# Kernel optimization log

Measured on AMD Instinct MI355X. Metric: run time of the kernel, lower is better.

## Reference

```python
import jax, jax.numpy as jnp
import numpy as np

B, P, H, W = 8, 128, 32, 32
NC = 4                 # num_classes = NUM_REL_GROUP + 1
DOBJ = 4424            # 2*DOBJ = 8848
CIN = 256
C = 128 + 8848         # 8976 GCN channel dim


def setup_inputs() -> dict:
    key = jax.random.key(0)
    ks = jax.random.split(key, 24)
    s = 0.02  # weight scale to keep activations moderate
    inp = {
        "x": jax.random.normal(ks[0], (B, CIN, H, W), jnp.float32),
        "rel_pair_idxs": jax.random.randint(ks[1], (B, P, 2), 0, 640, dtype=jnp.int32),
        "obj_rep": jax.random.normal(ks[2], (640, DOBJ), jnp.float32),
        # ADD_GCN params
        "fc_w": jax.random.normal(ks[3], (NC, CIN), jnp.float32) * s,
        "ct_w": jax.random.normal(ks[4], (128, CIN), jnp.float32) * s,
        "ct_b": jnp.zeros((128,), jnp.float32),
        # DynamicGraphConvolution params
        "A": jax.random.normal(ks[5], (NC, NC), jnp.float32) * 0.25,          # static_adj conv1d (no bias)
        "sw_w": jax.random.normal(ks[6], (C, C), jnp.float32) * s / np.sqrt(C) * 30,
        "sw_b": jnp.zeros((C,), jnp.float32),
        "cg_w": jax.random.normal(ks[7], (C, C), jnp.float32) * s / np.sqrt(C) * 30,
        "cg_b": jnp.zeros((C,), jnp.float32),
        "bn_g": jnp.ones((C,), jnp.float32),
        "bn_b": jnp.zeros((C,), jnp.float32),
        "bn_m": jnp.zeros((C,), jnp.float32),
        "bn_v": jnp.ones((C,), jnp.float32),
        "co_w": jax.random.normal(ks[8], (NC, 2 * C), jnp.float32) * s / np.sqrt(C) * 30,
        "co_b": jnp.zeros((NC,), jnp.float32),
        "dw_w": jax.random.normal(ks[9], (C, C), jnp.float32) * s / np.sqrt(C) * 30,
        "dw_b": jnp.zeros((C,), jnp.float32),
        "ll_w": jax.random.normal(ks[10], (NC, C), jnp.float32) * s / np.sqrt(C) * 30,
        "ll_b": jnp.zeros((NC,), jnp.float32),
        "mask_mat": jnp.eye(NC, dtype=jnp.float32),
    }
    return inp


def reference(x, rel_pair_idxs, obj_rep, fc_w, ct_w, ct_b, A, sw_w, sw_b,
              cg_w, cg_b, bn_g, bn_b, bn_m, bn_v, co_w, co_b, dw_w, dw_b,
              ll_w, ll_b, mask_mat):
    leaky = lambda t: jax.nn.leaky_relu(t, 0.2)
    b, cin, h, w = x.shape
    xr = x.reshape(b, cin, h * w)                                  # (B,256,HW)

    # forward_classification_sm: fc -> topk(1).mean == max over spatial
    y = jnp.einsum('oc,bcs->bos', fc_w, xr)                        # (B,NC,HW)
    out1 = y.max(-1)                                               # (B,NC)

    # forward_sam
    mask = jax.nn.sigmoid(y)                                       # (B,NC,HW)
    v = jnp.einsum('oc,bcs->bos', ct_w, xr) + ct_b[None, :, None]  # (B,128,HW)
    v = jnp.einsum('bcs,bns->bcn', v, mask)                        # (B,128,NC)

    # pairwise object features (gather), tiled over NC node slots
    o1 = obj_rep[rel_pair_idxs[..., 0]]                            # (B,P,DOBJ)
    o2 = obj_rep[rel_pair_idxs[..., 1]]
    pf = jnp.concatenate([o1, o2], -1)                             # (B,P,8848)
    p = pf.shape[1]
    pf = jnp.broadcast_to(pf[..., None], pf.shape + (NC,))         # (B,P,8848,NC)
    vb = jnp.broadcast_to(v[:, None], (b, p) + v.shape[1:])        # (B,P,128,NC)
    g = jnp.concatenate([pf, vb], 2).reshape(b * p, C, NC)         # (BP,C,NC)

    # --- DynamicGraphConvolution ---
    # static GCN: node-mix conv1d (no bias) + leaky, then channel 1x1 conv + leaky
    xs = leaky(jnp.einsum('nm,pcm->pcn', A, g))                    # (BP,C,NC)
    xs = leaky(jnp.einsum('oc,pcn->pon', sw_w, xs) + sw_b[None, :, None])
    hg = g + xs

    # dynamic adjacency
    glb = hg.mean(-1)                                              # (BP,C) gap
    glb = glb @ cg_w.T + cg_b                                      # conv_global (1x1)
    glb = (glb - bn_m) * jax.lax.rsqrt(bn_v + 1e-5) * bn_g + bn_b  # BN (eval)
    glb = leaky(glb)
    # conv_create_co_mat over cat([glb_expand, hg], ch) without materializing cat
    adj = jax.nn.sigmoid(
        jnp.einsum('oc,pc->po', co_w[:, :C], glb)[:, :, None]
        + jnp.einsum('oc,pcn->pon', co_w[:, C:], hg)
        + co_b[None, :, None])                                     # (BP,NC,NC)

    # dynamic GCN
    hd = leaky(jnp.einsum('pcn,pnm->pcm', hg, adj))
    z = leaky(jnp.einsum('oc,pcn->pon', dw_w, hd) + dw_b[None, :, None])  # (BP,C,NC)

    # head: last_linear + leaky, masked diagonal sum
    out2 = leaky(jnp.einsum('oc,pcn->pon', ll_w, z) + ll_b[None, :, None])  # (BP,NC,NC)
    out2 = (out2 * jax.lax.stop_gradient(mask_mat)).sum(-1)        # (BP,NC)

    o1b = jnp.broadcast_to(out1[:, None], (b, p, NC)).reshape(b * p, NC)
    return ((o1b + out2) * 0.5).reshape(b, p, NC)
```

## Files before the change

kernel.cpp:

```cpp
#include <hip/hip_runtime.h>
#include <stdint.h>

#define DEVI __device__ __forceinline__

typedef unsigned short u16;
typedef __bf16 bf16x8 __attribute__((ext_vector_type(8)));
typedef float f32x4 __attribute__((ext_vector_type(4)));
typedef u16 u16x8 __attribute__((ext_vector_type(8)));

DEVI u16 f2bf(float f){
  union { float f; unsigned u; } v; v.f = f;
  unsigned r = v.u + 0x7FFFu + ((v.u >> 16) & 1u);
  return (u16)(r >> 16);
}
DEVI float bf2f(u16 h){
  union { unsigned u; float f; } v; v.u = ((unsigned)h) << 16;
  return v.f;
}
DEVI float lky(float t){ return t > 0.f ? t : 0.2f * t; }

#define GLD16(gp, lp) __builtin_amdgcn_global_load_lds( \
    (const __attribute__((address_space(1))) void*)(gp), \
    (__attribute__((address_space(3))) void*)(lp), 16, 0, 0)


DEVI void stage_half(const u16* __restrict__ G, size_t grow0, int kcol, int Kp,
                     u16* lds, int t)
{
  #pragma unroll
  for (int j = 0; j < 2; ++j){
    const int off16 = j*512 + t;
    const int rl = off16 >> 3, sl = off16 & 7;
    const u16* gp = G + (grow0 + rl)*(size_t)Kp + kcol + ((sl ^ (rl & 7))*8);
    GLD16(gp, lds + off16*8);
  }
}

template<int RB, int RA>
DEVI void ph_reads(const u16* __restrict__ Ab, const u16* __restrict__ Bb,
                   bf16x8 (&afr)[4][2], bf16x8 (&bfr)[4][2],
                   int wr, int wc, int l4, int l15)
{
  if constexpr (RA >= 0){
    #pragma unroll
    for (int m = 0; m < 4; ++m){
      const int r = wr*128 + RA*64 + m*16 + l15;
      afr[m][0] = *(const bf16x8*)&Ab[r*64 + (((0+l4) ^ (r & 7))*8)];
      afr[m][1] = *(const bf16x8*)&Ab[r*64 + (((4+l4) ^ (r & 7))*8)];
    }
  }
  if constexpr (RB >= 0){
    #pragma unroll
    for (int nn = 0; nn < 2; ++nn){
      const int r = wc*64 + (RB+nn)*16 + l15;
      bfr[RB+nn][0] = *(const bf16x8*)&Bb[r*64 + (((0+l4) ^ (r & 7))*8)];
      bfr[RB+nn][1] = *(const bf16x8*)&Bb[r*64 + (((4+l4) ^ (r & 7))*8)];
    }
  }
}

template<int MH, int NH, int VM>
DEVI void ph_mfma(bf16x8 (&afr)[4][2], bf16x8 (&bfr)[4][2], f32x4 (&acc)[8][4])
{
  __builtin_amdgcn_s_barrier();
  __builtin_amdgcn_s_setprio(1);
  #pragma unroll
  for (int m = 0; m < 4; ++m)
    #pragma unroll
    for (int nn = 0; nn < 2; ++nn)
      #pragma unroll
      for (int ks = 0; ks < 2; ++ks)
        acc[MH*4+m][NH+nn] = __builtin_amdgcn_mfma_f32_16x16x32_bf16(
            afr[m][ks], bfr[NH+nn][ks], acc[MH*4+m][NH+nn], 0, 0, 0);
  __builtin_amdgcn_s_setprio(0);
  if constexpr (VM == 4){
    asm volatile("s_waitcnt vmcnt(4)" ::: "memory");
  }
  __builtin_amdgcn_s_barrier();
}

template<int EPI>
__global__ __launch_bounds__(512, 2)
void gemm256(const u16* __restrict__ A, const u16* __restrict__ B,
             int Kp, int Nt, int SN, int Mreal, float* __restrict__ C, long long ldc,
             const float* __restrict__ bias, const float* __restrict__ scale,
             const float* __restrict__ off, const float* __restrict__ llw,
             float* __restrict__ oacc)
{
  __shared__ __align__(16) u16 As[2][16384];
  __shared__ __align__(16) u16 Bs[2][16384];
  const int t    = threadIdx.x;
  const int lane = t & 63;
  const int wid  = t >> 6;
  const int wr = wid >> 2, wc = wid & 3;
  const int l4 = lane >> 4, l15 = lane & 15;

  const int nwg = gridDim.x;
  const int xc = blockIdx.x & 7, pp = blockIdx.x >> 3;
  const int qq = nwg >> 3, rr = nwg & 7;
  const int wg = (xc < rr ? xc*(qq+1) : rr*(qq+1) + (xc-rr)*qq) + pp;
  const int strip_sz = (nwg / Nt) * SN;
  const int strip = wg / strip_sz, srem = wg % strip_sz;
  const int mt = srem / SN, nt = strip*SN + srem % SN;

  const size_t am0 = (size_t)mt*256;
  const size_t bn0 = (size_t)nt*256;

  f32x4 acc[8][4];
  #pragma unroll
  for (int i = 0; i < 8; ++i)
    #pragma unroll
    for (int j = 0; j < 4; ++j) acc[i][j] = f32x4{0.f,0.f,0.f,0.f};
  bf16x8 afr[4][2], bfr[4][2];

  const int NT2 = Kp >> 6;
  const int NI  = NT2 >> 1;

  stage_half(A, am0+0,   0,  Kp, &As[0][0],    t);
  stage_half(A, am0+128, 0,  Kp, &As[0][8192], t);
  stage_half(B, bn0+0,   0,  Kp, &Bs[0][0],    t);
  stage_half(B, bn0+128, 0,  Kp, &Bs[0][8192], t);
  stage_half(B, bn0+0,   64, Kp, &Bs[1][0],    t);
  stage_half(B, bn0+128, 64, Kp, &Bs[1][8192], t);
  asm volatile("s_waitcnt vmcnt(4)" ::: "memory");
  __builtin_amdgcn_s_barrier();

  for (int i = 0; i < NI; ++i){
    const int k1  = 2*i + 1;
    const int ts0 = (2*i+2 < NT2) ? 2*i+2 : 2*i;
    const int ts1 = (2*i+3 < NT2) ? 2*i+3 : 2*i+1;
    ph_reads<0,0>(&As[0][0], &Bs[0][0], afr, bfr, wr, wc, l4, l15);
    stage_half(A, am0+0,   k1*64,  Kp, &As[1][0],    t);
    ph_mfma<0,0,-1>(afr, bfr, acc);
    ph_reads<2,-1>(&As[0][0], &Bs[0][0], afr, bfr, wr, wc, l4, l15);
    stage_half(A, am0+128, k1*64,  Kp, &As[1][8192], t);
    ph_mfma<0,2,-1>(afr, bfr, acc);
    ph_reads<-1,1>(&As[0][0], &Bs[0][0], afr, bfr, wr, wc, l4, l15);
    stage_half(B, bn0+0,   ts0*64, Kp, &Bs[0][0],    t);
    ph_mfma<1,2,-1>(afr, bfr, acc);
    stage_half(B, bn0+128, ts0*64, Kp, &Bs[0][8192], t);
    ph_mfma<1,0,4>(afr, bfr, acc);
    ph_reads<0,0>(&As[1][0], &Bs[1][0], afr, bfr, wr, wc, l4, l15);
    stage_half(A, am0+0,   ts0*64, Kp, &As[0][0],    t);
    ph_mfma<0,0,-1>(afr, bfr, acc);
    ph_reads<2,-1>(&As[1][0], &Bs[1][0], afr, bfr, wr, wc, l4, l15);
    stage_half(A, am0+128, ts0*64, Kp, &As[0][8192], t);
    ph_mfma<0,2,-1>(afr, bfr, acc);
    ph_reads<-1,1>(&As[1][0], &Bs[1][0], afr, bfr, wr, wc, l4, l15);
    stage_half(B, bn0+0,   ts1*64, Kp, &Bs[1][0],    t);
    ph_mfma<1,2,-1>(afr, bfr, acc);
    stage_half(B, bn0+128, ts1*64, Kp, &Bs[1][8192], t);
    ph_mfma<1,0,4>(afr, bfr, acc);
  }
  asm volatile("s_waitcnt vmcnt(0)" ::: "memory");

  const int ob0 = mt*256 + wr*128;
  const int nb0 = nt*256 + wc*64;

  if (EPI == 0){
    #pragma unroll
    for (int mi = 0; mi < 8; ++mi){
      const int ob = ob0 + mi*16 + l4*4;
      if (ob < Mreal){
        #pragma unroll
        for (int ni = 0; ni < 4; ++ni){
          const int n = nb0 + ni*16 + l15;
          *(f32x4*)&C[(size_t)n*ldc + ob] = acc[mi][ni];
        }
      }
    }
  } else if (EPI == 2){
    #pragma unroll
    for (int mi = 0; mi < 8; ++mi){
      const int ob = ob0 + mi*16 + l4*4;
      if (ob < Mreal){
        const float sc0=scale[ob],sc1=scale[ob+1],sc2=scale[ob+2],sc3=scale[ob+3];
        const float of0=off[ob],of1=off[ob+1],of2=off[ob+2],of3=off[ob+3];
        #pragma unroll
        for (int ni = 0; ni < 4; ++ni){
          const int n = nb0 + ni*16 + l15;
          f32x4 a = acc[mi][ni];
          f32x4 vv = { lky(a[0]*sc0+of0), lky(a[1]*sc1+of1),
                       lky(a[2]*sc2+of2), lky(a[3]*sc3+of3) };
          *(f32x4*)&C[(size_t)n*ldc + ob] = vv;
        }
      }
    }
  } else {
    #pragma unroll
    for (int ni = 0; ni < 4; ++ni){
      float s0=0.f, s1=0.f, s2=0.f, s3=0.f;
      #pragma unroll
      for (int mi = 0; mi < 8; ++mi){
        #pragma unroll
        for (int r = 0; r < 4; ++r){
          const int o = ob0 + mi*16 + l4*4 + r;
          if (o < Mreal){
            const float val = lky(acc[mi][ni][r] + bias[o]);
            s0 += llw[o]         * val;
            s1 += llw[8976 + o]  * val;
            s2 += llw[17952 + o] * val;
            s3 += llw[26928 + o] * val;
          }
        }
      }
      const int n = nb0 + ni*16 + l15;
      const int q = n >> 2, m = n & 3;
      float sv[4] = {s0,s1,s2,s3};
      #pragma unroll
      for (int o4 = 0; o4 < 4; ++o4){
        float tt = sv[o4];
        tt += __shfl_xor(tt, 16);
        tt += __shfl_xor(tt, 32);
        if (l4 == 0) atomicAdd(&oacc[(q*4 + o4)*4 + m], tt);
      }
    }
  }
}

__global__ __launch_bounds__(256)
void gemm_vpre(const u16* __restrict__ A, const u16* __restrict__ B,
               int Kp, int Nt, int Mreal, float* __restrict__ C, long long ldc,
               const float* __restrict__ bias)
{
  __shared__ __align__(16) u16 As[2][4096];
  __shared__ __align__(16) u16 Bs[2][4096];
  const int tid  = threadIdx.x;
  const int lane = tid & 63;
  const int wr   = (tid >> 6) >> 1, wc = (tid >> 6) & 1;
  const int l4   = lane >> 4, l15 = lane & 15;
  const int mt   = blockIdx.x / Nt, nt = blockIdx.x % Nt;

  const size_t arow = (size_t)(mt*128 + (tid>>2)) * Kp + (tid&3)*8;
  const size_t brow = (size_t)(nt*128 + (tid>>2)) * Kp + (tid&3)*8;
  const int    ldst = (tid>>2)*32 + (tid&3)*8;
  const size_t rowskip = (size_t)64 * Kp;

  f32x4 acc[4][4];
  #pragma unroll
  for (int i=0;i<4;i++)
    #pragma unroll
    for (int j=0;j<4;j++) acc[i][j] = f32x4{0.f,0.f,0.f,0.f};

  const int NT = Kp >> 5;
  {
    const u16* a0 = A + arow; const u16* b0 = B + brow;
    GLD16(a0,           &As[0][ldst]);
    GLD16(a0 + rowskip, &As[0][ldst + 2048]);
    GLD16(b0,           &Bs[0][ldst]);
    GLD16(b0 + rowskip, &Bs[0][ldst + 2048]);
  }
  __syncthreads();

  for (int kt=0; kt<NT; ++kt){
    const int cur = kt & 1;
    if (kt + 1 < NT){
      const u16* a0 = A + arow + (size_t)(kt+1)*32;
      const u16* b0 = B + brow + (size_t)(kt+1)*32;
      GLD16(a0,           &As[cur^1][ldst]);
      GLD16(a0 + rowskip, &As[cur^1][ldst + 2048]);
      GLD16(b0,           &Bs[cur^1][ldst]);
      GLD16(b0 + rowskip, &Bs[cur^1][ldst + 2048]);
    }
    bf16x8 af[4], bf[4];
    #pragma unroll
    for (int mi=0;mi<4;mi++)
      af[mi] = *(const bf16x8*)&As[cur][(wr*64 + mi*16 + l15)*32 + l4*8];
    #pragma unroll
    for (int ni=0;ni<4;ni++)
      bf[ni] = *(const bf16x8*)&Bs[cur][(wc*64 + ni*16 + l15)*32 + l4*8];
    #pragma unroll
    for (int mi=0;mi<4;mi++)
      #pragma unroll
      for (int ni=0;ni<4;ni++)
        acc[mi][ni] = __builtin_amdgcn_mfma_f32_16x16x32_bf16(af[mi], bf[ni], acc[mi][ni], 0, 0, 0);
    __syncthreads();
  }

  const int ob0 = mt*128 + wr*64;
  const int nb0 = nt*128 + wc*64;
  #pragma unroll
  for (int mi=0;mi<4;mi++)
    #pragma unroll
    for (int r=0;r<4;r++){
      const int o = ob0 + mi*16 + l4*4 + r;
      if (o < Mreal){
        const float bb = bias[o];
        #pragma unroll
        for (int ni=0;ni<4;ni++){
          const int n = nb0 + ni*16 + l15;
          C[(size_t)o*ldc + n] = acc[mi][ni][r] + bb;
        }
      }
    }
}

__global__ void k_cvt_pad(const float* __restrict__ src, int srows, int scols,
                          int lds_, int koff, u16* __restrict__ dst, int Kp)
{
  const int r = blockIdx.x;
  const int nch = Kp >> 3;
  for (int ch = threadIdx.x; ch < nch; ch += blockDim.x){
    const int k = ch*8;
    u16 o[8];
    if (r < srows){
      #pragma unroll
      for (int i=0;i<8;i++){
        const int kk = k + i;
        o[i] = (kk < scols) ? f2bf(src[(size_t)r*lds_ + koff + kk]) : (u16)0;
      }
    } else {
      #pragma unroll
      for (int i=0;i<8;i++) o[i] = 0;
    }
    u16x8 vv = { o[0],o[1],o[2],o[3],o[4],o[5],o[6],o[7] };
    *(u16x8*)&dst[(size_t)r*Kp + k] = vv;
  }
}

__global__ void k_cvt_sww(const float* __restrict__ src, u16* __restrict__ dst)
{
  const int r = blockIdx.x;
  const float* row = src + (size_t)r*8976;
  u16* d1 = dst + (size_t)r*4480;
  u16* d2 = dst + (size_t)(8976+r)*4480;
  for (int ch = threadIdx.x; ch < 560; ch += 256){
    const int k = ch*8;
    u16 a[8], b[8];
    #pragma unroll
    for (int i=0;i<8;i++){
      const int kk = k+i;
      a[i] = (kk < 4424) ? f2bf(row[kk])        : (u16)0;
      b[i] = (kk < 4424) ? f2bf(row[4424 + kk]) : (u16)0;
    }
    u16x8 va = { a[0],a[1],a[2],a[3],a[4],a[5],a[6],a[7] };
    u16x8 vb = { b[0],b[1],b[2],b[3],b[4],b[5],b[6],b[7] };
    *(u16x8*)&d1[k] = va;
    *(u16x8*)&d2[k] = vb;
  }
}

__global__ void k_cvt_obj(const float* __restrict__ obj, u16* __restrict__ dst)
{
  const int r = blockIdx.x;
  const int ab = (r >= 640);
  const float* src = obj + (size_t)(ab ? r-640 : r)*4424;
  for (int ch = threadIdx.x; ch < 560; ch += 256){
    const int k = ch*8;
    u16 o[8];
    #pragma unroll
    for (int i=0;i<8;i++){
      const int kk = k+i;
      float f = (kk < 4424) ? src[kk] : 0.f;
      if (ab) f = fabsf(f);
      o[i] = f2bf(f);
    }
    u16x8 vv = { o[0],o[1],o[2],o[3],o[4],o[5],o[6],o[7] };
    *(u16x8*)&dst[(size_t)r*4480 + k] = vv;
  }
}

__global__ void k_xT(const float* __restrict__ x, u16* __restrict__ xT)
{
  __shared__ float t[32][33];
  const int bid = blockIdx.x;
  const int b = bid >> 8; const int cs = (bid >> 5) & 7; const int ss = bid & 31;
  const int tx = threadIdx.x & 31, ty = threadIdx.x >> 5;
  #pragma unroll
  for (int i=0;i<4;i++){
    const int r = ty + i*8;
    t[r][tx] = x[((size_t)(b*256 + cs*32 + r))*1024 + ss*32 + tx];
  }
  __syncthreads();
  #pragma unroll
  for (int i=0;i<4;i++){
    const int r = ty + i*8;
    xT[((size_t)(b*1024 + ss*32 + r))*256 + cs*32 + tx] = f2bf(t[tx][r]);
  }
}

__global__ void k_ymask(const float* __restrict__ x, const float* __restrict__ fcw,
                        float* __restrict__ y, float* __restrict__ mask)
{
  __shared__ float fc[1024];
  const int b = blockIdx.x >> 2, st = blockIdx.x & 3;
  for (int i=threadIdx.x; i<1024; i+=256) fc[i] = fcw[i];
  __syncthreads();
  const int s = st*256 + threadIdx.x;
  float a0=0,a1=0,a2=0,a3=0;
  for (int c=0;c<256;c++){
    const float xv = x[((size_t)(b*256+c))*1024 + s];
    a0 += fc[c]*xv; a1 += fc[256+c]*xv; a2 += fc[512+c]*xv; a3 += fc[768+c]*xv;
  }
  const size_t base = (size_t)(b*4)*1024 + s;
  y[base]        = a0; mask[base]        = 1.f/(1.f+expf(-a0));
  y[base+1024]   = a1; mask[base+1024]   = 1.f/(1.f+expf(-a1));
  y[base+2048]   = a2; mask[base+2048]   = 1.f/(1.f+expf(-a2));
  y[base+3072]   = a3; mask[base+3072]   = 1.f/(1.f+expf(-a3));
}

__global__ void k_out1(const float* __restrict__ y, float* __restrict__ out1){
  const int bn = blockIdx.x;
  float m = -3.4e38f;
  for (int s=threadIdx.x; s<1024; s+=256) m = fmaxf(m, y[(size_t)bn*1024+s]);
  for (int o=32;o;o>>=1) m = fmaxf(m, __shfl_xor(m,o));
  __shared__ float red[4];
  if ((threadIdx.x&63)==0) red[threadIdx.x>>6] = m;
  __syncthreads();
  if (threadIdx.x==0) out1[bn] = fmaxf(fmaxf(red[0],red[1]),fmaxf(red[2],red[3]));
}

__global__ void k_v(const float* __restrict__ vpreT, const float* __restrict__ mask,
                    float* __restrict__ v){
  const int b = blockIdx.x >> 7, j = blockIdx.x & 127;
  float a[4]={0,0,0,0};
  for (int s=threadIdx.x; s<1024; s+=256){
    const float pv = vpreT[(size_t)j*8192 + b*1024 + s];
    #pragma unroll
    for (int m=0;m<4;m++) a[m] += pv * mask[((size_t)(b*4+m))*1024 + s];
  }
  __shared__ float red[4][5];
  #pragma unroll
  for (int m=0;m<4;m++){
    float t=a[m];
    for (int o=32;o;o>>=1) t += __shfl_xor(t,o);
    if ((threadIdx.x&63)==0) red[m][threadIdx.x>>6]=t;
  }
  __syncthreads();
  if (threadIdx.x<4)
    v[(size_t)(b*128+j)*4 + threadIdx.x] =
      red[threadIdx.x][0]+red[threadIdx.x][1]+red[threadIdx.x][2]+red[threadIdx.x][3];
}

__global__ void k_lv(const float* __restrict__ Am, const float* __restrict__ v,
                     float* __restrict__ lv){
  const int idx = blockIdx.x*256 + threadIdx.x;
  if (idx < 1024){
    #pragma unroll
    for (int n=0;n<4;n++){
      float s=0;
      #pragma unroll
      for (int m=0;m<4;m++) s += Am[n*4+m]*v[idx*4+m];
      lv[idx*4+n] = lky(s);
    }
  }
}

__global__ void k_sV(const float* __restrict__ sw, const float* __restrict__ lv,
                     float* __restrict__ sV){
  __shared__ float l[4096];
  for (int i=threadIdx.x; i<4096; i+=256) l[i]=lv[i];
  __syncthreads();
  const int o = blockIdx.x*256 + threadIdx.x;
  if (o >= 8976) return;
  float acc[8][4] = {};
  const float* row = sw + (size_t)o*8976 + 8848;
  for (int j=0;j<128;j++){
    const float wv = row[j];
    #pragma unroll
    for (int b=0;b<8;b++){
      const float* lb = &l[(b*128+j)*4];
      #pragma unroll
      for (int n=0;n<4;n++) acc[b][n] += wv*lb[n];
    }
  }
  #pragma unroll
  for (int b=0;b<8;b++){
    f32x4 vv = {acc[b][0],acc[b][1],acc[b][2],acc[b][3]};
    *(f32x4*)&sV[((size_t)b*8976 + o)*4] = vv;
  }
}

__global__ void k_so(const float* __restrict__ cgb, const float* __restrict__ g,
                     const float* __restrict__ b2, const float* __restrict__ m,
                     const float* __restrict__ vvar, float* __restrict__ so){
  const int o = blockIdx.x*256+threadIdx.x;
  if (o<8976){
    const float sc = g[o]*rsqrtf(vvar[o]+1e-5f);
    so[o]=sc; so[8976+o] = (cgb[o]-m[o])*sc + b2[o];
  }
}

__global__ void k_glb_t2(const float* __restrict__ U, const float* __restrict__ obj,
                         const int* __restrict__ rel,
                         const float* __restrict__ sV, const float* __restrict__ swb,
                         const float* __restrict__ v, const float* __restrict__ Am,
                         const float* __restrict__ cow, u16* __restrict__ glbB,
                         float* __restrict__ t2)
{
  const int q = blockIdx.x; const int b = q >> 7;
  const int i1 = rel[q*2], i2 = rel[q*2+1];
  const float* u1  = U + (size_t)i1*17952;
  const float* u2  = U + (size_t)i2*17952 + 8976;
  const float* u1a = U + (size_t)(640+i1)*17952;
  const float* u2a = U + (size_t)(640+i2)*17952 + 8976;
  const float* o1 = obj + (size_t)i1*4424;
  const float* o2 = obj + (size_t)i2*4424;
  float rA[4], aA[4];
  #pragma unroll
  for (int n=0;n<4;n++){
    const float s = Am[n*4]+Am[n*4+1]+Am[n*4+2]+Am[n*4+3];
    rA[n]=0.6f*s; aA[n]=0.4f*fabsf(s);
  }
  float t2a[16] = {};
  for (int c = threadIdx.x; c < 9088; c += 256){
    if (c < 8976){
      const float p1 = u1[c] + u2[c];
      const float p2 = u1a[c] + u2a[c];
      const f32x4 sv = *(const f32x4*)&sV[((size_t)b*8976 + c)*4];
      const float sb = swb[c];
      const float gs = (c < 4424) ? o1[c] : (c < 8848) ? o2[c-4424] : 0.f;
      float hg[4]; float sum = 0.f;
      #pragma unroll
      for (int n=0;n<4;n++){
        const float xs2 = lky(rA[n]*p1 + aA[n]*p2 + sv[n] + sb);
        const float g = (c < 8848) ? gs : v[((size_t)b*128 + (c-8848))*4 + n];
        hg[n] = g + xs2; sum += hg[n];
      }
      glbB[(size_t)q*9088 + c] = f2bf(0.25f*sum);
      #pragma unroll
      for (int o4=0;o4<4;o4++){
        const float cw = cow[(size_t)o4*17952 + 8976 + c];
        #pragma unroll
        for (int n=0;n<4;n++) t2a[o4*4+n] += cw*hg[n];
      }
    } else {
      glbB[(size_t)q*9088 + c] = 0;
    }
  }
  __shared__ float red[16][5];
  #pragma unroll
  for (int i=0;i<16;i++){
    float t = t2a[i];
    for (int o=32;o;o>>=1) t += __shfl_xor(t,o);
    if ((threadIdx.x&63)==0) red[i][threadIdx.x>>6]=t;
  }
  __syncthreads();
  if (threadIdx.x < 16)
    t2[q*16+threadIdx.x] = red[threadIdx.x][0]+red[threadIdx.x][1]
                          +red[threadIdx.x][2]+red[threadIdx.x][3];
}

__global__ void k_adj(const float* __restrict__ glb2, const float* __restrict__ cow,
                      const float* __restrict__ t2, const float* __restrict__ cob,
                      float* __restrict__ adj)
{
  const int q = blockIdx.x;
  float a[4]={0,0,0,0};
  for (int c=threadIdx.x; c<8976; c+=256){
    const float g = glb2[(size_t)q*8976+c];
    #pragma unroll
    for (int o=0;o<4;o++) a[o] += cow[(size_t)o*17952 + c]*g;
  }
  __shared__ float red[4][5]; __shared__ float co1[4];
  #pragma unroll
  for (int i=0;i<4;i++){
    float t=a[i]; for (int o=32;o;o>>=1) t += __shfl_xor(t,o);
    if ((threadIdx.x&63)==0) red[i][threadIdx.x>>6]=t;
  }
  __syncthreads();
  if (threadIdx.x<4)
    co1[threadIdx.x]=red[threadIdx.x][0]+red[threadIdx.x][1]+red[threadIdx.x][2]+red[threadIdx.x][3];
  __syncthreads();
  if (threadIdx.x<16){
    const int a_=threadIdx.x>>2, m=threadIdx.x&3;
    const float t = co1[a_] + t2[q*16 + a_*4 + m] + cob[a_];
    adj[q*16 + a_*4 + m] = 1.f/(1.f+expf(-t));
  }
}

__global__ void k_hd(const float* __restrict__ U, const float* __restrict__ obj,
                     const int* __restrict__ rel,
                     const float* __restrict__ sV, const float* __restrict__ swb,
                     const float* __restrict__ v, const float* __restrict__ Am,
                     const float* __restrict__ adj, u16* __restrict__ hdb)
{
  const int q = blockIdx.x; const int b = q>>7;
  const int i1 = rel[q*2], i2 = rel[q*2+1];
  const float* u1  = U + (size_t)i1*17952;
  const float* u2  = U + (size_t)i2*17952 + 8976;
  const float* u1a = U + (size_t)(640+i1)*17952;
  const float* u2a = U + (size_t)(640+i2)*17952 + 8976;
  const float* o1 = obj + (size_t)i1*4424;
  const float* o2 = obj + (size_t)i2*4424;
  float rA[4], aA[4];
  #pragma unroll
  for (int n=0;n<4;n++){
    const float s = Am[n*4]+Am[n*4+1]+Am[n*4+2]+Am[n*4+3];
    rA[n]=0.6f*s; aA[n]=0.4f*fabsf(s);
  }
  __shared__ float aj[16];
  if (threadIdx.x<16) aj[threadIdx.x] = adj[q*16+threadIdx.x];
  __syncthreads();
  float ajr[16];
  #pragma unroll
  for (int i=0;i<16;i++) ajr[i]=aj[i];
  for (int c=threadIdx.x; c<9088; c+=256){
    if (c<8976){
      const float p1 = u1[c] + u2[c];
      const float p2 = u1a[c] + u2a[c];
      const f32x4 sv = *(const f32x4*)&sV[((size_t)b*8976 + c)*4];
      const float sb = swb[c];
      const float gs = (c < 4424) ? o1[c] : (c < 8848) ? o2[c-4424] : 0.f;
      float hg[4];
      #pragma unroll
      for (int n=0;n<4;n++){
        const float xs2 = lky(rA[n]*p1 + aA[n]*p2 + sv[n] + sb);
        const float g = (c < 8848) ? gs : v[((size_t)b*128 + (c-8848))*4 + n];
        hg[n] = g + xs2;
      }
      #pragma unroll
      for (int m=0;m<4;m++){
        const float hv = lky(hg[0]*ajr[m] + hg[1]*ajr[4+m] + hg[2]*ajr[8+m] + hg[3]*ajr[12+m]);
        hdb[((size_t)(q*4+m))*9088 + c] = f2bf(hv);
      }
    } else {
      #pragma unroll
      for (int m=0;m<4;m++) hdb[((size_t)(q*4+m))*9088 + c] = 0;
    }
  }
}

__global__ void k_final(const float* __restrict__ o2f, const float* __restrict__ out1,
                        const float* __restrict__ llb, const float* __restrict__ mm,
                        float* __restrict__ out)
{
  const int idx = blockIdx.x*256+threadIdx.x;
  if (idx < 4096){
    const int q = idx>>2, o = idx&3, b = q>>7;
    float s=0.f;
    #pragma unroll
    for (int m=0;m<4;m++) s += lky(o2f[(q*4+o)*4+m] + llb[o]) * mm[o*4+m];
    out[idx] = 0.5f*(out1[b*4+o] + s);
  }
}

extern "C" void kernel_launch(void* const* d_in, const int* in_sizes, int n_in,
                              void* d_out, int out_size, void* d_ws, size_t ws_size,
                              hipStream_t stream)
{
  const float* x    = (const float*)d_in[0];
  const int*   rel  = (const int*)d_in[1];
  const float* obj  = (const float*)d_in[2];
  const float* fcw  = (const float*)d_in[3];
  const float* ctw  = (const float*)d_in[4];
  const float* ctb  = (const float*)d_in[5];
  const float* Am   = (const float*)d_in[6];
  const float* sww  = (const float*)d_in[7];
  const float* swb  = (const float*)d_in[8];
  const float* cgw  = (const float*)d_in[9];
  const float* cgb  = (const float*)d_in[10];
  const float* bng  = (const float*)d_in[11];
  const float* bnb  = (const float*)d_in[12];
  const float* bnm  = (const float*)d_in[13];
  const float* bnv  = (const float*)d_in[14];
  const float* cow  = (const float*)d_in[15];
  const float* cob  = (const float*)d_in[16];
  const float* dww  = (const float*)d_in[17];
  const float* dwb  = (const float*)d_in[18];
  const float* llw  = (const float*)d_in[19];
  const float* llb  = (const float*)d_in[20];
  const float* mm   = (const float*)d_in[21];
  float* out = (float*)d_out;
  (void)in_sizes; (void)n_in; (void)out_size; (void)ws_size;

  char* ws = (char*)d_ws;
  size_t off = 0;
  auto alloc = [&](size_t bytes)->char*{
    char* p = ws + off; off = (off + bytes + 255) & ~(size_t)255; return p;
  };
  u16*   Wb    = (u16*)  alloc((size_t)9216*9088*2);
  float* U     = (float*)alloc((size_t)1280*17952*4);
  u16*   glbB  = (u16*)  alloc((size_t)1024*9088*2);
  u16*   hdb   = (u16*)  alloc((size_t)4096*9088*2);
  u16*   objB  = (u16*)  alloc((size_t)1280*4480*2);
  float* glb2  = (float*)alloc((size_t)1024*8976*4);
  u16*   xT    = (u16*)  alloc((size_t)8192*256*2);
  u16*   ctwb  = (u16*)  alloc((size_t)128*256*2);
  float* y     = (float*)alloc((size_t)32768*4);
  float* mask  = (float*)alloc((size_t)32768*4);
  float* out1  = (float*)alloc((size_t)32*4);
  float* vpreT = (float*)alloc((size_t)128*8192*4);
  float* v     = (float*)alloc((size_t)4096*4);
  float* lv    = (float*)alloc((size_t)4096*4);
  float* sV    = (float*)alloc((size_t)287232*4);
  float* so    = (float*)alloc((size_t)2*8976*4);
  float* t2    = (float*)alloc((size_t)16384*4);
  float* adj   = (float*)alloc((size_t)16384*4);
  float* o2f   = (float*)alloc((size_t)16384*4);

  k_xT<<<dim3(2048), dim3(256), 0, stream>>>(x, xT);
  k_cvt_pad<<<dim3(128), dim3(256), 0, stream>>>(ctw, 128, 256, 256, 0, ctwb, 256);
  k_ymask<<<dim3(32), dim3(256), 0, stream>>>(x, fcw, y, mask);
  k_out1<<<dim3(32), dim3(256), 0, stream>>>(y, out1);
  gemm_vpre<<<dim3(64), dim3(256), 0, stream>>>(
      ctwb, xT, 256, 64, 128, vpreT, (long long)8192, ctb);
  k_v<<<dim3(1024), dim3(256), 0, stream>>>(vpreT, mask, v);

  k_cvt_obj<<<dim3(1280), dim3(256), 0, stream>>>(obj, objB);
  k_cvt_sww<<<dim3(8976), dim3(256), 0, stream>>>(sww, Wb);
  gemm256<0><<<dim3(71*5), dim3(512), 0, stream>>>(
      Wb, objB, 4480, 5, 5, 17952, U, (long long)17952,
      nullptr, nullptr, nullptr, nullptr, nullptr);

  k_lv<<<dim3(4), dim3(256), 0, stream>>>(Am, v, lv);
  k_sV<<<dim3(36), dim3(256), 0, stream>>>(sww, lv, sV);
  k_glb_t2<<<dim3(1024), dim3(256), 0, stream>>>(U, obj, rel, sV, swb, v, Am,
                                                 cow, glbB, t2);

  k_cvt_pad<<<dim3(9216), dim3(256), 0, stream>>>(cgw, 8976, 8976, 8976, 0, Wb, 9088);
  k_so<<<dim3(36), dim3(256), 0, stream>>>(cgb, bng, bnb, bnm, bnv, so);
  gemm256<2><<<dim3(36*4), dim3(512), 0, stream>>>(
      Wb, glbB, 9088, 4, 4, 8976, glb2, (long long)8976,
      nullptr, so, so + 8976, nullptr, nullptr);

  k_adj<<<dim3(1024), dim3(256), 0, stream>>>(glb2, cow, t2, cob, adj);
  k_cvt_pad<<<dim3(9216), dim3(256), 0, stream>>>(dww, 8976, 8976, 8976, 0, Wb, 9088);
  k_hd<<<dim3(1024), dim3(256), 0, stream>>>(U, obj, rel, sV, swb, v, Am, adj, hdb);

  hipMemsetAsync(o2f, 0, (size_t)16384*4, stream);
  gemm256<3><<<dim3(36*16), dim3(512), 0, stream>>>(
      Wb, hdb, 9088, 16, 8, 8976, nullptr, 0, dwb,
      nullptr, nullptr, llw, o2f);

  k_final<<<dim3(16), dim3(256), 0, stream>>>(o2f, out1, llb, mm, out);
}
```

Measured before the change: 2.118 ms.

## Replace 8-wave 256x256 GEMM with 16-wave K32 double-buffered variant

Rewrites the shared bf16 GEMM kernel to run 1024 threads (16 waves) per 256x256 tile, each wave owning a 64x64 sub-tile, with a K-step of 32 and a simple two-buffer LDS ping-pong. This halves LDS use and register accumulators per wave, aiming for higher occupancy and simpler scheduling. In exchange, it drops the phased interleaving of loads and MFMAs. It now waits for all outstanding loads and hits a barrier every 32-wide K step, which can expose global load latency and add synchronisation overhead.

```diff
diff --git a/kernel.cpp b/kernel.cpp
--- a/kernel.cpp
+++ b/kernel.cpp
@@ -23,72 +23,16 @@
     (const __attribute__((address_space(1))) void*)(gp), \
     (__attribute__((address_space(3))) void*)(lp), 16, 0, 0)
 
-
-DEVI void stage_half(const u16* __restrict__ G, size_t grow0, int kcol, int Kp,
-                     u16* lds, int t)
-{
-  #pragma unroll
-  for (int j = 0; j < 2; ++j){
-    const int off16 = j*512 + t;
-    const int rl = off16 >> 3, sl = off16 & 7;
-    const u16* gp = G + (grow0 + rl)*(size_t)Kp + kcol + ((sl ^ (rl & 7))*8);
-    GLD16(gp, lds + off16*8);
-  }
-}
-
-template<int RB, int RA>
-DEVI void ph_reads(const u16* __restrict__ Ab, const u16* __restrict__ Bb,
-                   bf16x8 (&afr)[4][2], bf16x8 (&bfr)[4][2],
-                   int wr, int wc, int l4, int l15)
-{
-  if constexpr (RA >= 0){
-    #pragma unroll
-    for (int m = 0; m < 4; ++m){
-      const int r = wr*128 + RA*64 + m*16 + l15;
-      afr[m][0] = *(const bf16x8*)&Ab[r*64 + (((0+l4) ^ (r & 7))*8)];
-      afr[m][1] = *(const bf16x8*)&Ab[r*64 + (((4+l4) ^ (r & 7))*8)];
-    }
-  }
-  if constexpr (RB >= 0){
-    #pragma unroll
-    for (int nn = 0; nn < 2; ++nn){
-      const int r = wc*64 + (RB+nn)*16 + l15;
-      bfr[RB+nn][0] = *(const bf16x8*)&Bb[r*64 + (((0+l4) ^ (r & 7))*8)];
-      bfr[RB+nn][1] = *(const bf16x8*)&Bb[r*64 + (((4+l4) ^ (r & 7))*8)];
-    }
-  }
-}
-
-template<int MH, int NH, int VM>
-DEVI void ph_mfma(bf16x8 (&afr)[4][2], bf16x8 (&bfr)[4][2], f32x4 (&acc)[8][4])
-{
-  __builtin_amdgcn_s_barrier();
-  __builtin_amdgcn_s_setprio(1);
-  #pragma unroll
-  for (int m = 0; m < 4; ++m)
-    #pragma unroll
-    for (int nn = 0; nn < 2; ++nn)
-      #pragma unroll
-      for (int ks = 0; ks < 2; ++ks)
-        acc[MH*4+m][NH+nn] = __builtin_amdgcn_mfma_f32_16x16x32_bf16(
-            afr[m][ks], bfr[NH+nn][ks], acc[MH*4+m][NH+nn], 0, 0, 0);
-  __builtin_amdgcn_s_setprio(0);
-  if constexpr (VM == 4){
-    asm volatile("s_waitcnt vmcnt(4)" ::: "memory");
-  }
-  __builtin_amdgcn_s_barrier();
-}
-
 template<int EPI>
-__global__ __launch_bounds__(512, 2)
-void gemm256(const u16* __restrict__ A, const u16* __restrict__ B,
-             int Kp, int Nt, int SN, int Mreal, float* __restrict__ C, long long ldc,
-             const float* __restrict__ bias, const float* __restrict__ scale,
-             const float* __restrict__ off, const float* __restrict__ llw,
-             float* __restrict__ oacc)
-{
-  __shared__ __align__(16) u16 As[2][16384];
-  __shared__ __align__(16) u16 Bs[2][16384];
+__global__ __launch_bounds__(1024, 4)
+void gemmT(const u16* __restrict__ A, const u16* __restrict__ B,
+           int Kp, int Nt, int SN, int Mreal, float* __restrict__ C, long long ldc,
+           const float* __restrict__ bias, const float* __restrict__ scale,
+           const float* __restrict__ off, const float* __restrict__ llw,
+           float* __restrict__ oacc)
+{
+  __shared__ __align__(16) u16 As[2][8192];
+  __shared__ __align__(16) u16 Bs[2][8192];
   const int t    = threadIdx.x;
   const int lane = t & 63;
   const int wid  = t >> 6;
@@ -106,60 +50,71 @@
   const size_t am0 = (size_t)mt*256;
   const size_t bn0 = (size_t)nt*256;
 
-  f32x4 acc[8][4];
-  #pragma unroll
-  for (int i = 0; i < 8; ++i)
+  f32x4 acc[4][4];
+  #pragma unroll
+  for (int i = 0; i < 4; ++i)
     #pragma unroll
     for (int j = 0; j < 4; ++j) acc[i][j] = f32x4{0.f,0.f,0.f,0.f};
-  bf16x8 afr[4][2], bfr[4][2];
-
-  const int NT2 = Kp >> 6;
-  const int NI  = NT2 >> 1;
-
-  stage_half(A, am0+0,   0,  Kp, &As[0][0],    t);
-  stage_half(A, am0+128, 0,  Kp, &As[0][8192], t);
-  stage_half(B, bn0+0,   0,  Kp, &Bs[0][0],    t);
-  stage_half(B, bn0+128, 0,  Kp, &Bs[0][8192], t);
-  stage_half(B, bn0+0,   64, Kp, &Bs[1][0],    t);
-  stage_half(B, bn0+128, 64, Kp, &Bs[1][8192], t);
-  asm volatile("s_waitcnt vmcnt(4)" ::: "memory");
+  bf16x8 afr[4], bfr[4];
+
+  const int NT = Kp >> 5;
+
+  const int srl = t >> 2, ssl = t & 3;
+  const u16* pA = A + (am0 + srl)*(size_t)Kp + ((ssl ^ (srl & 3))*8);
+  const u16* pB = B + (bn0 + srl)*(size_t)Kp + ((ssl ^ (srl & 3))*8);
+
+  int aoff[4], boff[4];
+  #pragma unroll
+  for (int mi = 0; mi < 4; ++mi){
+    const int r = wr*64 + mi*16 + l15;
+    aoff[mi] = r*32 + ((l4 ^ (r & 3))*8);
+  }
+  #pragma unroll
+  for (int ni = 0; ni < 4; ++ni){
+    const int r = wc*64 + ni*16 + l15;
+    boff[ni] = r*32 + ((l4 ^ (r & 3))*8);
+  }
+
+  GLD16(pA, &As[0][0] + t*8);
+  GLD16(pB, &Bs[0][0] + t*8);
+  asm volatile("s_waitcnt vmcnt(0)" ::: "memory");
   __builtin_amdgcn_s_barrier();
 
-  for (int i = 0; i < NI; ++i){
-    const int k1  = 2*i + 1;
-    const int ts0 = (2*i+2 < NT2) ? 2*i+2 : 2*i;
-    const int ts1 = (2*i+3 < NT2) ? 2*i+3 : 2*i+1;
-    ph_reads<0,0>(&As[0][0], &Bs[0][0], afr, bfr, wr, wc, l4, l15);
-    stage_half(A, am0+0,   k1*64,  Kp, &As[1][0],    t);
-    ph_mfma<0,0,-1>(afr, bfr, acc);
-    ph_reads<2,-1>(&As[0][0], &Bs[0][0], afr, bfr, wr, wc, l4, l15);
-    stage_half(A, am0+128, k1*64,  Kp, &As[1][8192], t);
-    ph_mfma<0,2,-1>(afr, bfr, acc);
-    ph_reads<-1,1>(&As[0][0], &Bs[0][0], afr, bfr, wr, wc, l4, l15);
-    stage_half(B, bn0+0,   ts0*64, Kp, &Bs[0][0],    t);
-    ph_mfma<1,2,-1>(afr, bfr, acc);
-    stage_half(B, bn0+128, ts0*64, Kp, &Bs[0][8192], t);
-    ph_mfma<1,0,4>(afr, bfr, acc);
-    ph_reads<0,0>(&As[1][0], &Bs[1][0], afr, bfr, wr, wc, l4, l15);
-    stage_half(A, am0+0,   ts0*64, Kp, &As[0][0],    t);
-    ph_mfma<0,0,-1>(afr, bfr, acc);
-    ph_reads<2,-1>(&As[1][0], &Bs[1][0], afr, bfr, wr, wc, l4, l15);
-    stage_half(A, am0+128, ts0*64, Kp, &As[0][8192], t);
-    ph_mfma<0,2,-1>(afr, bfr, acc);
-    ph_reads<-1,1>(&As[1][0], &Bs[1][0], afr, bfr, wr, wc, l4, l15);
-    stage_half(B, bn0+0,   ts1*64, Kp, &Bs[1][0],    t);
-    ph_mfma<1,2,-1>(afr, bfr, acc);
-    stage_half(B, bn0+128, ts1*64, Kp, &Bs[1][8192], t);
-    ph_mfma<1,0,4>(afr, bfr, acc);
-  }
-  asm volatile("s_waitcnt vmcnt(0)" ::: "memory");
-
-  const int ob0 = mt*256 + wr*128;
+  #define GT_BODY(KT, RB_, WB_)                                              \
+  {                                                                          \
+    const int nx = ((KT)+1 < NT) ? (KT)+1 : NT-1;                            \
+    GLD16(pA + (size_t)nx*32, &As[WB_][0] + t*8);                            \
+    GLD16(pB + (size_t)nx*32, &Bs[WB_][0] + t*8);                            \
+    const u16* ab = &As[RB_][0];                                             \
+    const u16* bb = &Bs[RB_][0];                                             \
+    _Pragma("unroll")                                                        \
+    for (int mi = 0; mi < 4; ++mi) afr[mi] = *(const bf16x8*)&ab[aoff[mi]];  \
+    _Pragma("unroll")                                                        \
+    for (int ni = 0; ni < 4; ++ni) bfr[ni] = *(const bf16x8*)&bb[boff[ni]];  \
+    __builtin_amdgcn_s_setprio(1);                                           \
+    _Pragma("unroll")                                                        \
+    for (int mi = 0; mi < 4; ++mi)                                           \
+      _Pragma("unroll")                                                      \
+      for (int ni = 0; ni < 4; ++ni)                                         \
+        acc[mi][ni] = __builtin_amdgcn_mfma_f32_16x16x32_bf16(               \
+            afr[mi], bfr[ni], acc[mi][ni], 0, 0, 0);                         \
+    __builtin_amdgcn_s_setprio(0);                                           \
+    asm volatile("s_waitcnt vmcnt(0)" ::: "memory");                         \
+    __builtin_amdgcn_s_barrier();                                            \
+  }
+
+  for (int kt = 0; kt < NT; kt += 2){
+    GT_BODY(kt,   0, 1);
+    GT_BODY(kt+1, 1, 0);
+  }
+  #undef GT_BODY
+
+  const int ob0 = mt*256 + wr*64;
   const int nb0 = nt*256 + wc*64;
 
   if (EPI == 0){
     #pragma unroll
-    for (int mi = 0; mi < 8; ++mi){
+    for (int mi = 0; mi < 4; ++mi){
       const int ob = ob0 + mi*16 + l4*4;
       if (ob < Mreal){
         #pragma unroll
@@ -171,7 +126,7 @@
     }
   } else if (EPI == 2){
     #pragma unroll
-    for (int mi = 0; mi < 8; ++mi){
+    for (int mi = 0; mi < 4; ++mi){
       const int ob = ob0 + mi*16 + l4*4;
       if (ob < Mreal){
         const float sc0=scale[ob],sc1=scale[ob+1],sc2=scale[ob+2],sc3=scale[ob+3];
@@ -191,7 +146,7 @@
     for (int ni = 0; ni < 4; ++ni){
       float s0=0.f, s1=0.f, s2=0.f, s3=0.f;
       #pragma unroll
-      for (int mi = 0; mi < 8; ++mi){
+      for (int mi = 0; mi < 4; ++mi){
         #pragma unroll
         for (int r = 0; r < 4; ++r){
           const int o = ob0 + mi*16 + l4*4 + r;
@@ -699,7 +654,7 @@
 
   k_cvt_obj<<<dim3(1280), dim3(256), 0, stream>>>(obj, objB);
   k_cvt_sww<<<dim3(8976), dim3(256), 0, stream>>>(sww, Wb);
-  gemm256<0><<<dim3(71*5), dim3(512), 0, stream>>>(
+  gemmT<0><<<dim3(71*5), dim3(1024), 0, stream>>>(
       Wb, objB, 4480, 5, 5, 17952, U, (long long)17952,
       nullptr, nullptr, nullptr, nullptr, nullptr);
 
@@ -710,7 +665,7 @@
 
   k_cvt_pad<<<dim3(9216), dim3(256), 0, stream>>>(cgw, 8976, 8976, 8976, 0, Wb, 9088);
   k_so<<<dim3(36), dim3(256), 0, stream>>>(cgb, bng, bnb, bnm, bnv, so);
-  gemm256<2><<<dim3(36*4), dim3(512), 0, stream>>>(
+  gemmT<2><<<dim3(36*4), dim3(1024), 0, stream>>>(
       Wb, glbB, 9088, 4, 4, 8976, glb2, (long long)8976,
       nullptr, so, so + 8976, nullptr, nullptr);
 
@@ -719,7 +674,7 @@
   k_hd<<<dim3(1024), dim3(256), 0, stream>>>(U, obj, rel, sV, swb, v, Am, adj, hdb);
 
   hipMemsetAsync(o2f, 0, (size_t)16384*4, stream);
-  gemm256<3><<<dim3(36*16), dim3(512), 0, stream>>>(
+  gemmT<3><<<dim3(36*16), dim3(1024), 0, stream>>>(
       Wb, hdb, 9088, 16, 8, 8976, nullptr, 0, dwb,
       nullptr, nullptr, llw, o2f);
 
```

Result: slower. 2.289 ms (+8.1%).
